# Performance work log

Measured on AMD Instinct MI355X. Metric: run time of the kernel, lower is better.

The kernel has to match this reference:

```python
import jax, jax.numpy as jnp
import numpy as np

# Dims: B=batch, S=max_input_len (memory), T=max_output_len-1 (decode steps),
# V=vocab, E=embedding_dim, U=dec_units, M=encoder/memory feature dim (=U here).

def setup_inputs() -> dict:
    B, S, T, V, E, U, M = 64, 1024, 511, 1024, 512, 1024, 1024
    key = jax.random.key(0)
    ks = jax.random.split(key, 16)
    sc = 0.02
    return {
        "tokens": jax.random.randint(ks[0], (B, T), 0, V),
        "memory": jax.random.normal(ks[1], (B, S, M), jnp.float32),
        "enc_h": jax.random.normal(ks[2], (B, U), jnp.float32) * 0.1,
        "enc_c": jax.random.normal(ks[3], (B, U), jnp.float32) * 0.1,
        "emb": jax.random.normal(ks[4], (V, E), jnp.float32) * sc,
        # LSTM cell: input = concat(embedded token, prev attention) -> E+U
        "Wk": jax.random.normal(ks[5], (E + U, 4 * U), jnp.float32) * sc,
        "Wr": jax.random.normal(ks[6], (U, 4 * U), jnp.float32) * sc,
        "b": jnp.zeros((4 * U,), jnp.float32),
        # Bahdanau attention: memory layer, query layer, score vector v
        "Wm": jax.random.normal(ks[7], (M, U), jnp.float32) * sc,
        "Wq": jax.random.normal(ks[8], (U, U), jnp.float32) * sc,
        "v": jax.random.normal(ks[9], (U,), jnp.float32) * sc,
        # attention_layer (Dense, no bias): concat(cell_out, context) -> U
        "Wa": jax.random.normal(ks[10], (U + M, U), jnp.float32) * sc,
        # output projection fc
        "Wfc": jax.random.normal(ks[11], (U, V), jnp.float32) * sc,
        "bfc": jnp.zeros((V,), jnp.float32),
    }


def reference(tokens, memory, enc_h, enc_c, emb, Wk, Wr, b, Wm, Wq, v, Wa, Wfc, bfc):
    B, U = enc_h.shape
    # Precompute attention keys once (memory_layer applied to memory): [B,S,U]
    keys = jnp.einsum('bsm,mu->bsu', memory, Wm)
    # Embedded decoder inputs, time-major for scan: [T,B,E]
    xseq = jnp.transpose(emb[tokens], (1, 0, 2))
    attn0 = jnp.zeros((B, U), memory.dtype)

    def step(carry, x_t):
        h, c, attn = carry
        # AttentionWrapper: cell input = concat(input, prev attention)
        z = jnp.concatenate([x_t, attn], axis=-1) @ Wk + h @ Wr + b
        i, f, g, o = jnp.split(z, 4, axis=-1)  # keras gate order i,f,c,o
        i = jax.nn.sigmoid(i)
        f = jax.nn.sigmoid(f)
        g = jnp.tanh(g)
        o = jax.nn.sigmoid(o)
        c_new = f * c + i * g
        h_new = o * jnp.tanh(c_new)
        # Bahdanau additive score: v^T tanh(W_q h + keys) -> [B,S]
        q = h_new @ Wq
        score = jnp.einsum('bsu,u->bs', jnp.tanh(q[:, None, :] + keys), v)
        alig = jax.nn.softmax(score, axis=-1)  # full-length memory mask (all valid)
        ctx = jnp.einsum('bs,bsm->bm', alig, memory)
        # attention_layer (no bias, no activation)
        attn_new = jnp.concatenate([h_new, ctx], axis=-1) @ Wa
        # output_attention=True: fc applied to attention output
        out = attn_new @ Wfc + bfc
        return (h_new, c_new, attn_new), out

    _, outs = jax.lax.scan(step, (enc_h, enc_c, attn0), xseq)
    return jnp.transpose(outs, (1, 0, 2))  # [B,T,V] rnn_output logits
```

## Files before the change

kernel.cpp:

```cpp
#include <hip/hip_runtime.h>
#include <stdint.h>

#define BB 64
#define SS 1024
#define TT 511
#define EE 512
#define UU 1024
#define G4 4096

typedef __bf16 bf16x8 __attribute__((ext_vector_type(8)));
typedef float  f32x4  __attribute__((ext_vector_type(4)));
typedef unsigned short u16x8 __attribute__((ext_vector_type(8)));

__device__ __forceinline__ float bf2f_lo(unsigned int u) {
    union { unsigned int i; float f; } w; w.i = u << 16; return w.f;
}
__device__ __forceinline__ float bf2f_hi(unsigned int u) {
    union { unsigned int i; float f; } w; w.i = u & 0xFFFF0000u; return w.f;
}
__device__ __forceinline__ unsigned short f2bf(float f) {
    union { float f; unsigned int i; } w; w.f = f;
    return (unsigned short)((w.i + 0x7FFFu + ((w.i >> 16) & 1u)) >> 16);
}
__device__ __forceinline__ float bfu2f(unsigned short u) {
    union { unsigned int i; float f; } w; w.i = ((unsigned int)u) << 16; return w.f;
}
__device__ __forceinline__ float fast_tanh(float x) {
    float e = __expf(2.0f * x);
    return 1.0f - 2.0f / (e + 1.0f);
}
__device__ __forceinline__ float sigmoidf_(float x) {
    return 1.0f / (1.0f + __expf(-x));
}

__device__ __forceinline__ int frag_slot(int m, int k, int KT, int hl) {
    return ((((m >> 4) * KT + (k >> 5)) * 2 + hl) * 64
            + ((m & 15) + (((k >> 3) & 3) << 4))) * 8 + (k & 7);
}

__device__ __forceinline__ f32x4 mfma16(bf16x8 a, bf16x8 b, f32x4 c) {
    return __builtin_amdgcn_mfma_f32_16x16x32_bf16(a, b, c, 0, 0, 0);
}

__global__ void k_cvt(const float4* __restrict__ src, ushort4* __restrict__ dst, int n4)
{
    int idx = blockIdx.x * 256 + threadIdx.x;
    for (int i = idx; i < n4; i += (int)gridDim.x * 256) {
        float4 f = src[i];
        ushort4 o;
        o.x = f2bf(f.x); o.y = f2bf(f.y); o.z = f2bf(f.z); o.w = f2bf(f.w);
        dst[i] = o;
    }
}

template<int OUTBF16>
__global__ __launch_bounds__(256) void k_mm1024(const float* __restrict__ A,
                                                const float* __restrict__ W,
                                                unsigned short* __restrict__ obf,
                                                float* __restrict__ of32)
{
    __shared__ __align__(16) float As[32][68];
    __shared__ __align__(16) float Ws[32][72];
    const int tid = threadIdx.x;
    const int tx = tid & 15, ty = tid >> 4;
    const int r0 = blockIdx.y * 64;
    const int c0 = blockIdx.x * 64;
    float acc[4][4] = {};
    const int am = tid >> 2, akq = tid & 3;
    const int wc4 = (tid & 15) * 4, wk0 = tid >> 4;
    for (int k0 = 0; k0 < 1024; k0 += 32) {
        const float* p = A + (size_t)(r0 + am) * 1024 + k0 + 8 * akq;
        float4 x0 = *(const float4*)p;
        float4 x1 = *(const float4*)(p + 4);
        As[8*akq+0][am] = x0.x; As[8*akq+1][am] = x0.y; As[8*akq+2][am] = x0.z; As[8*akq+3][am] = x0.w;
        As[8*akq+4][am] = x1.x; As[8*akq+5][am] = x1.y; As[8*akq+6][am] = x1.z; As[8*akq+7][am] = x1.w;
        #pragma unroll
        for (int j = 0; j < 2; ++j) {
            const int kk = wk0 + 16 * j;
            *(float4*)&Ws[kk][wc4] = *(const float4*)&W[(size_t)(k0 + kk) * 1024 + c0 + wc4];
        }
        __syncthreads();
        #pragma unroll
        for (int kk = 0; kk < 32; ++kk) {
            float4 a4 = *(const float4*)&As[kk][4 * ty];
            float4 w4 = *(const float4*)&Ws[kk][4 * tx];
            const float aa[4] = {a4.x, a4.y, a4.z, a4.w};
            const float ww[4] = {w4.x, w4.y, w4.z, w4.w};
            #pragma unroll
            for (int i = 0; i < 4; ++i)
                #pragma unroll
                for (int j = 0; j < 4; ++j)
                    acc[i][j] += aa[i] * ww[j];
        }
        __syncthreads();
    }
    #pragma unroll
    for (int i = 0; i < 4; ++i)
        #pragma unroll
        for (int j = 0; j < 4; ++j) {
            const size_t o = (size_t)(r0 + 4*ty + i) * 1024 + c0 + 4*tx + j;
            if (OUTBF16) obf[o] = f2bf(acc[i][j]);
            else         of32[o] = acc[i][j];
        }
}

__global__ void k_packw(const float* __restrict__ W1, const float* __restrict__ W2,
                        int split, int nmode, int KT, int s1, int s2,
                        unsigned short* __restrict__ dst)
{
    const int gid = blockIdx.x * 256 + threadIdx.x;
    const int lane = gid & 63;
    const int rest = gid >> 6;
    const int kt = rest % KT, nt = rest / KT;
    const int n = nt * 16 + (lane & 15);
    const int k0 = kt * 32 + (((lane >> 4) & 3) << 3);
    u16x8 hi, lo;
    #pragma unroll
    for (int j = 0; j < 8; ++j) {
        const int k = k0 + j;
        float f;
        if (nmode) f = (n < split) ? W1[(size_t)k * s1 + n] : W2[(size_t)k * s2 + (n - split)];
        else       f = (k < split) ? W1[(size_t)k * s1 + n] : W2[(size_t)(k - split) * s2 + n];
        hi[j] = f2bf(f);
        lo[j] = f2bf(f - bfu2f(hi[j]));
    }
    u16x8* d8 = (u16x8*)dst;
    d8[((nt * KT + kt) * 2 + 0) * 64 + lane] = hi;
    d8[((nt * KT + kt) * 2 + 1) * 64 + lane] = lo;
}

__global__ void k_init2(const float* __restrict__ enc_h, const float* __restrict__ enc_c,
                        const float* __restrict__ emb, const int* __restrict__ tokens,
                        float* __restrict__ c, unsigned short* __restrict__ Az)
{
    const int idx = blockIdx.x * 256 + threadIdx.x;
    const int b = idx >> 10, u = idx & 1023;
    c[idx] = enc_c[idx];
    const float hv = enc_h[idx];
    const unsigned short hh = f2bf(hv);
    const unsigned short hl = f2bf(hv - bfu2f(hh));
    Az[frag_slot(b, 1536 + u, 80, 0)] = hh;
    Az[frag_slot(b, 1536 + u, 80, 1)] = hl;
    Az[frag_slot(b, 512 + u, 80, 0)] = 0;
    Az[frag_slot(b, 512 + u, 80, 1)] = 0;
    if (u < EE) {
        const int tok = tokens[b * TT];
        const float v = emb[(size_t)tok * EE + u];
        const unsigned short eh = f2bf(v);
        Az[frag_slot(b, u, 80, 0)] = eh;
        Az[frag_slot(b, u, 80, 1)] = f2bf(v - bfu2f(eh));
    }
}

__global__ __launch_bounds__(256, 4) void k_mfma_z(const unsigned short* __restrict__ Azp,
                                                   const unsigned short* __restrict__ Bpp,
                                                   float* __restrict__ zpart)
{
    __shared__ float red[4][16][64];
    const int lane = threadIdx.x & 63, w = threadIdx.x >> 6;
    const int nt = blockIdx.x;
    const int g  = blockIdx.y;
    const bf16x8* A = (const bf16x8*)Azp;
    const bf16x8* B = (const bf16x8*)Bpp;
    f32x4 acc[4] = {{0.f,0.f,0.f,0.f},{0.f,0.f,0.f,0.f},{0.f,0.f,0.f,0.f},{0.f,0.f,0.f,0.f}};
    const int kt0 = g * 20 + w * 5;
    #pragma unroll
    for (int kk = 0; kk < 5; ++kk) {
        const int kt = kt0 + kk;
        const bf16x8 bh = B[((nt * 80 + kt) * 2 + 0) * 64 + lane];
        const bf16x8 bl = B[((nt * 80 + kt) * 2 + 1) * 64 + lane];
        #pragma unroll
        for (int m = 0; m < 4; ++m) {
            const bf16x8 ah = A[((m * 80 + kt) * 2 + 0) * 64 + lane];
            const bf16x8 al = A[((m * 80 + kt) * 2 + 1) * 64 + lane];
            acc[m] = mfma16(al, bh, acc[m]);
            acc[m] = mfma16(ah, bl, acc[m]);
            acc[m] = mfma16(ah, bh, acc[m]);
        }
    }
    #pragma unroll
    for (int m = 0; m < 4; ++m)
        #pragma unroll
        for (int r = 0; r < 4; ++r)
            red[w][m * 4 + r][lane] = acc[m][r];
    __syncthreads();
    const int m = w;
    float* Z = zpart + (size_t)g * BB * G4;
    const int col = nt * 16 + (lane & 15);
    const int rbase = (lane >> 4) * 4;
    #pragma unroll
    for (int r = 0; r < 4; ++r) {
        const float s = red[0][m*4+r][lane] + red[1][m*4+r][lane]
                      + red[2][m*4+r][lane] + red[3][m*4+r][lane];
        Z[(size_t)(m * 16 + rbase + r) * G4 + col] = s;
    }
}

__global__ __launch_bounds__(256, 4) void k_mfma_q(const unsigned short* __restrict__ Aqp,
                                                   const unsigned short* __restrict__ Bpp,
                                                   float* __restrict__ qpart)
{
    __shared__ float red[4][16][64];
    const int lane = threadIdx.x & 63, w = threadIdx.x >> 6;
    const int nt = blockIdx.x;
    const int g  = blockIdx.y;
    const bf16x8* A = (const bf16x8*)Aqp;
    const bf16x8* B = (const bf16x8*)Bpp;
    f32x4 acc[4] = {{0.f,0.f,0.f,0.f},{0.f,0.f,0.f,0.f},{0.f,0.f,0.f,0.f},{0.f,0.f,0.f,0.f}};
    const int kt0 = g * 8 + w * 2;
    #pragma unroll
    for (int kk = 0; kk < 2; ++kk) {
        const int kt = kt0 + kk;
        const bf16x8 bh = B[((nt * 32 + kt) * 2 + 0) * 64 + lane];
        const bf16x8 bl = B[((nt * 32 + kt) * 2 + 1) * 64 + lane];
        #pragma unroll
        for (int m = 0; m < 4; ++m) {
            const bf16x8 ah = A[((m * 32 + kt) * 2 + 0) * 64 + lane];
            const bf16x8 al = A[((m * 32 + kt) * 2 + 1) * 64 + lane];
            acc[m] = mfma16(al, bh, acc[m]);
            acc[m] = mfma16(ah, bl, acc[m]);
            acc[m] = mfma16(ah, bh, acc[m]);
        }
    }
    #pragma unroll
    for (int m = 0; m < 4; ++m)
        #pragma unroll
        for (int r = 0; r < 4; ++r)
            red[w][m * 4 + r][lane] = acc[m][r];
    __syncthreads();
    const int m = w;
    float* Q = qpart + (size_t)g * BB * UU;
    const int col = nt * 16 + (lane & 15);
    const int rbase = (lane >> 4) * 4;
    #pragma unroll
    for (int r = 0; r < 4; ++r) {
        const float s = red[0][m*4+r][lane] + red[1][m*4+r][lane]
                      + red[2][m*4+r][lane] + red[3][m*4+r][lane];
        Q[(size_t)(m * 16 + rbase + r) * UU + col] = s;
    }
}

__global__ __launch_bounds__(512, 2) void k_mfma_comb(const unsigned short* __restrict__ Aap,
                                                      const unsigned short* __restrict__ Bpp,
                                                      unsigned short* __restrict__ Az,
                                                      float* __restrict__ out,
                                                      const float* __restrict__ bfc, int t)
{
    __shared__ float red[8][16][64];
    const int lane = threadIdx.x & 63, w = threadIdx.x >> 6;
    const int nt = blockIdx.x;
    const bf16x8* A = (const bf16x8*)Aap;
    const bf16x8* B = (const bf16x8*)Bpp;
    f32x4 acc[4] = {{0.f,0.f,0.f,0.f},{0.f,0.f,0.f,0.f},{0.f,0.f,0.f,0.f},{0.f,0.f,0.f,0.f}};
    const int kt0 = w * 8;
    #pragma unroll
    for (int kk = 0; kk < 8; ++kk) {
        const int kt = kt0 + kk;
        const bf16x8 bh = B[((nt * 64 + kt) * 2 + 0) * 64 + lane];
        const bf16x8 bl = B[((nt * 64 + kt) * 2 + 1) * 64 + lane];
        #pragma unroll
        for (int m = 0; m < 4; ++m) {
            const bf16x8 ah = A[((m * 64 + kt) * 2 + 0) * 64 + lane];
            const bf16x8 al = A[((m * 64 + kt) * 2 + 1) * 64 + lane];
            acc[m] = mfma16(al, bh, acc[m]);
            acc[m] = mfma16(ah, bl, acc[m]);
            acc[m] = mfma16(ah, bh, acc[m]);
        }
    }
    #pragma unroll
    for (int m = 0; m < 4; ++m)
        #pragma unroll
        for (int r = 0; r < 4; ++r)
            red[w][m * 4 + r][lane] = acc[m][r];
    __syncthreads();
    if (w >= 4) return;
    const int m = w;
    const int n = nt * 16 + (lane & 15);
    const int rbase = (lane >> 4) * 4;
    #pragma unroll
    for (int r = 0; r < 4; ++r) {
        float s = 0.f;
        #pragma unroll
        for (int ww = 0; ww < 8; ++ww) s += red[ww][m*4+r][lane];
        const int row = m * 16 + rbase + r;
        if (n < 1024) {
            const unsigned short hh = f2bf(s);
            Az[frag_slot(row, 512 + n, 80, 0)] = hh;
            Az[frag_slot(row, 512 + n, 80, 1)] = f2bf(s - bfu2f(hh));
        } else {
            const int col = n - 1024;
            out[((size_t)row * TT + t) * 1024 + col] = s + bfc[col];
        }
    }
}

__global__ void k_gates2(const float* __restrict__ zpart, const float* __restrict__ bias,
                         float* __restrict__ c, unsigned short* __restrict__ Aq,
                         unsigned short* __restrict__ Aa2, unsigned short* __restrict__ Az,
                         const float* __restrict__ emb, const int* __restrict__ tokens,
                         int tnext)
{
    const int idx = blockIdx.x * 256 + threadIdx.x;
    if (idx < BB * UU) {
        const int b = idx >> 10, u = idx & 1023;
        float zi = 0.f, zf = 0.f, zg = 0.f, zo = 0.f;
        #pragma unroll
        for (int p = 0; p < 4; ++p) {
            const float* zp = zpart + ((size_t)p * BB + b) * G4;
            zi += zp[u]; zf += zp[u + 1024]; zg += zp[u + 2048]; zo += zp[u + 3072];
        }
        const float i_ = sigmoidf_(zi + bias[u]);
        const float f_ = sigmoidf_(zf + bias[u + 1024]);
        const float g_ = fast_tanh(zg + bias[u + 2048]);
        const float o_ = sigmoidf_(zo + bias[u + 3072]);
        const float cn = f_ * c[idx] + i_ * g_;
        c[idx] = cn;
        const float hv = o_ * fast_tanh(cn);
        const unsigned short hh = f2bf(hv);
        const unsigned short hl = f2bf(hv - bfu2f(hh));
        Aq [frag_slot(b, u,        32, 0)] = hh;  Aq [frag_slot(b, u,        32, 1)] = hl;
        Aa2[frag_slot(b, u,        64, 0)] = hh;  Aa2[frag_slot(b, u,        64, 1)] = hl;
        Az [frag_slot(b, 1536 + u, 80, 0)] = hh;  Az [frag_slot(b, 1536 + u, 80, 1)] = hl;
    } else if (tnext < TT) {
        const int r = idx - BB * UU;
        const int lane = r & 63;
        const int kt = (r >> 6) & 15;
        const int mrep = r >> 10;
        const int bb = mrep * 16 + (lane & 15);
        const int k0 = kt * 32 + (((lane >> 4) & 3) << 3);
        const int tok = tokens[bb * TT + tnext];
        const float* e = emb + (size_t)tok * EE + k0;
        const float4 x0 = *(const float4*)e;
        const float4 x1 = *(const float4*)(e + 4);
        const float f[8] = {x0.x, x0.y, x0.z, x0.w, x1.x, x1.y, x1.z, x1.w};
        u16x8 hi, lo;
        #pragma unroll
        for (int j = 0; j < 8; ++j) {
            hi[j] = f2bf(f[j]);
            lo[j] = f2bf(f[j] - bfu2f(hi[j]));
        }
        u16x8* A8 = (u16x8*)Az;
        A8[((mrep * 80 + kt) * 2 + 0) * 64 + lane] = hi;
        A8[((mrep * 80 + kt) * 2 + 1) * 64 + lane] = lo;
    }
}

__global__ void k_packctx(const float* __restrict__ ctxpart, const float* __restrict__ denompart,
                          unsigned short* __restrict__ Aa2)
{
    __shared__ float rdsh;
    const int idx = blockIdx.x * 256 + threadIdx.x;
    const int b = idx >> 10, u = idx & 1023;
    if (threadIdx.x == 0) {
        float d = 0.f;
        #pragma unroll
        for (int ch = 0; ch < 16; ++ch) d += denompart[ch * BB + b];
        rdsh = 1.0f / d;
    }
    float v = 0.f;
    #pragma unroll
    for (int ch = 0; ch < 16; ++ch) v += ctxpart[((size_t)ch * BB + b) * UU + u];
    __syncthreads();
    v *= rdsh;
    const unsigned short hh = f2bf(v);
    Aa2[frag_slot(b, 1024 + u, 64, 0)] = hh;
    Aa2[frag_slot(b, 1024 + u, 64, 1)] = f2bf(v - bfu2f(hh));
}

template<int BF16>
__global__ __launch_bounds__(256) void k_attn(const unsigned short* __restrict__ keys,
        const void* __restrict__ mem, const float* __restrict__ qpart,
        const float* __restrict__ vvec, float* __restrict__ denompart,
        float* __restrict__ ctxpart)
{
    __shared__ float qs[1024];
    __shared__ float vs[1024];
    __shared__ float es[64];
    __shared__ float dsum[4];
    __shared__ __align__(16) float cred[128][8];
    const int tid = threadIdx.x;
    const int bid = blockIdx.x;
    const int b = bid >> 4, chunk = bid & 15;
    const int s0 = chunk * 64;
    for (int i = tid; i < UU; i += 256) {
        const size_t o = (size_t)b * UU + i;
        qs[i] = qpart[o] + qpart[o + (size_t)BB * UU]
              + qpart[o + 2 * (size_t)BB * UU] + qpart[o + 3 * (size_t)BB * UU];
        vs[i] = vvec[i];
    }
    __syncthreads();
    const int lane = tid & 63;
    const int w = tid >> 6;
    float qv[16], vv[16];
    #pragma unroll
    for (int j = 0; j < 2; ++j)
        #pragma unroll
        for (int i = 0; i < 8; ++i) {
            qv[8*j + i] = qs[8*lane + 512*j + i];
            vv[8*j + i] = vs[8*lane + 512*j + i];
        }
    float wsum = 0.f;
    for (int it = 0; it < 8; ++it) {
        const int sl = w * 16 + it * 2;
        const unsigned short* kp0 = keys + ((size_t)(b * SS + s0 + sl) << 10);
        const unsigned short* kp1 = kp0 + 1024;
        const uint4 r00 = *(const uint4*)&kp0[8*lane];
        const uint4 r01 = *(const uint4*)&kp0[8*lane + 512];
        const uint4 r10 = *(const uint4*)&kp1[8*lane];
        const uint4 r11 = *(const uint4*)&kp1[8*lane + 512];
        float acc0 = 0.f, acc1 = 0.f;
        {
            const uint4 rr[2] = {r00, r01};
            #pragma unroll
            for (int j = 0; j < 2; ++j) {
                float kx[8];
                kx[0] = bf2f_lo(rr[j].x); kx[1] = bf2f_hi(rr[j].x);
                kx[2] = bf2f_lo(rr[j].y); kx[3] = bf2f_hi(rr[j].y);
                kx[4] = bf2f_lo(rr[j].z); kx[5] = bf2f_hi(rr[j].z);
                kx[6] = bf2f_lo(rr[j].w); kx[7] = bf2f_hi(rr[j].w);
                #pragma unroll
                for (int i = 0; i < 8; ++i)
                    acc0 += vv[8*j + i] * fast_tanh(qv[8*j + i] + kx[i]);
            }
        }
        {
            const uint4 rr[2] = {r10, r11};
            #pragma unroll
            for (int j = 0; j < 2; ++j) {
                float kx[8];
                kx[0] = bf2f_lo(rr[j].x); kx[1] = bf2f_hi(rr[j].x);
                kx[2] = bf2f_lo(rr[j].y); kx[3] = bf2f_hi(rr[j].y);
                kx[4] = bf2f_lo(rr[j].z); kx[5] = bf2f_hi(rr[j].z);
                kx[6] = bf2f_lo(rr[j].w); kx[7] = bf2f_hi(rr[j].w);
                #pragma unroll
                for (int i = 0; i < 8; ++i)
                    acc1 += vv[8*j + i] * fast_tanh(qv[8*j + i] + kx[i]);
            }
        }
        #pragma unroll
        for (int m = 32; m >= 1; m >>= 1) {
            acc0 += __shfl_xor(acc0, m, 64);
            acc1 += __shfl_xor(acc1, m, 64);
        }
        if (lane == 0) {
            const float e0 = __expf(acc0);
            const float e1 = __expf(acc1);
            es[sl] = e0;
            es[sl + 1] = e1;
            wsum += e0 + e1;
        }
    }
    if (lane == 0) dsum[w] = wsum;
    __syncthreads();
    if (tid == 0)
        denompart[chunk * BB + b] = dsum[0] + dsum[1] + dsum[2] + dsum[3];
    const int m8 = (tid & 127) * 8;
    const int shalf = tid >> 7;
    float a[8] = {};
    #pragma unroll 8
    for (int i = 0; i < 32; ++i) {
        const int sl = shalf * 32 + i;
        const float wgt = es[sl];
        const size_t base = ((size_t)(b * SS + s0 + sl) << 10) + m8;
        if (BF16) {
            uint4 u = *(const uint4*)((const unsigned short*)mem + base);
            a[0] += wgt * bf2f_lo(u.x); a[1] += wgt * bf2f_hi(u.x);
            a[2] += wgt * bf2f_lo(u.y); a[3] += wgt * bf2f_hi(u.y);
            a[4] += wgt * bf2f_lo(u.z); a[5] += wgt * bf2f_hi(u.z);
            a[6] += wgt * bf2f_lo(u.w); a[7] += wgt * bf2f_hi(u.w);
        } else {
            const float* fp = (const float*)mem + base;
            const float4 f0 = *(const float4*)fp;
            const float4 f1 = *(const float4*)(fp + 4);
            a[0] += wgt * f0.x; a[1] += wgt * f0.y; a[2] += wgt * f0.z; a[3] += wgt * f0.w;
            a[4] += wgt * f1.x; a[5] += wgt * f1.y; a[6] += wgt * f1.z; a[7] += wgt * f1.w;
        }
    }
    if (shalf) {
        #pragma unroll
        for (int j = 0; j < 8; ++j) cred[tid - 128][j] = a[j];
    }
    __syncthreads();
    if (!shalf) {
        float* cp = ctxpart + ((size_t)chunk * BB + b) * UU + m8;
        float4 o0, o1;
        o0.x = a[0] + cred[tid][0]; o0.y = a[1] + cred[tid][1];
        o0.z = a[2] + cred[tid][2]; o0.w = a[3] + cred[tid][3];
        o1.x = a[4] + cred[tid][4]; o1.y = a[5] + cred[tid][5];
        o1.z = a[6] + cred[tid][6]; o1.w = a[7] + cred[tid][7];
        *(float4*)cp = o0;
        *(float4*)(cp + 4) = o1;
    }
}

extern "C" void kernel_launch(void* const* d_in, const int* in_sizes, int n_in,
                              void* d_out, int out_size, void* d_ws, size_t ws_size,
                              hipStream_t stream)
{
    const int*   tokens = (const int*)d_in[0];
    const float* memory = (const float*)d_in[1];
    const float* enc_h  = (const float*)d_in[2];
    const float* enc_c  = (const float*)d_in[3];
    const float* emb    = (const float*)d_in[4];
    const float* Wk     = (const float*)d_in[5];
    const float* Wr     = (const float*)d_in[6];
    const float* bias   = (const float*)d_in[7];
    const float* Wm     = (const float*)d_in[8];
    const float* Wq     = (const float*)d_in[9];
    const float* vvec   = (const float*)d_in[10];
    const float* Wa     = (const float*)d_in[11];
    const float* Wfc    = (const float*)d_in[12];
    const float* bfc    = (const float*)d_in[13];
    float* out = (float*)d_out;

    char* ws = (char*)d_ws;
    size_t off = 0;
    auto take = [&](size_t bytes) -> char* {
        char* p = ws + off;
        off = (off + bytes + 255) & ~(size_t)255;
        return p;
    };
    unsigned short* keys   = (unsigned short*)take((size_t)BB * SS * UU * 2);
    unsigned short* WkrP   = (unsigned short*)take((size_t)256 * 80 * 2 * 64 * 16);
    unsigned short* WcombP = (unsigned short*)take((size_t)128 * 64 * 2 * 64 * 16);
    unsigned short* WqP    = (unsigned short*)take((size_t)64  * 32 * 2 * 64 * 16);
    float* wafc  = (float*)take((size_t)2048 * 1024 * 4);
    float* zpart = (float*)take((size_t)4 * BB * G4 * 4);
    float* qpart = (float*)take((size_t)4 * BB * UU * 4);
    float* c     = (float*)take((size_t)BB * UU * 4);
    float* ctxpart   = (float*)take((size_t)16 * BB * UU * 4);
    float* denompart = (float*)take((size_t)16 * BB * 4);
    unsigned short* Az  = (unsigned short*)take((size_t)4 * 80 * 2 * 64 * 16);
    unsigned short* Aq  = (unsigned short*)take((size_t)4 * 32 * 2 * 64 * 16);
    unsigned short* Aa2 = (unsigned short*)take((size_t)4 * 64 * 2 * 64 * 16);
    const bool planA = (off + (size_t)BB * SS * UU * 2) <= ws_size;
    unsigned short* membf = planA ? (unsigned short*)take((size_t)BB * SS * UU * 2) : nullptr;

    k_init2<<<dim3(256), dim3(256), 0, stream>>>(enc_h, enc_c, emb, tokens, c, Az);
    if (planA)
        k_cvt<<<dim3(4096), dim3(256), 0, stream>>>((const float4*)memory, (ushort4*)membf,
                                                    (BB * SS * UU) / 4);
    k_mm1024<1><<<dim3(16, 1024), dim3(256), 0, stream>>>(memory, Wm, keys, nullptr);
    k_mm1024<0><<<dim3(16, 32),   dim3(256), 0, stream>>>(Wa, Wfc, nullptr, wafc);
    k_packw<<<dim3(5120), dim3(256), 0, stream>>>(Wk, Wr, 1536, 0, 80, 4096, 4096, WkrP);
    k_packw<<<dim3(512),  dim3(256), 0, stream>>>(Wq, Wq, 1 << 30, 0, 32, 1024, 1024, WqP);
    k_packw<<<dim3(2048), dim3(256), 0, stream>>>(Wa, wafc, 1024, 1, 64, 1024, 1024, WcombP);

    for (int t = 0; t < TT; ++t) {
        k_mfma_z<<<dim3(256, 4), dim3(256), 0, stream>>>(Az, WkrP, zpart);
        k_gates2<<<dim3(272), dim3(256), 0, stream>>>(zpart, bias, c, Aq, Aa2, Az,
                                                      emb, tokens, t + 1);
        k_mfma_q<<<dim3(64, 4), dim3(256), 0, stream>>>(Aq, WqP, qpart);
        if (planA)
            k_attn<1><<<dim3(1024), dim3(256), 0, stream>>>(keys, membf, qpart, vvec,
                                                            denompart, ctxpart);
        else
            k_attn<0><<<dim3(1024), dim3(256), 0, stream>>>(keys, memory, qpart, vvec,
                                                            denompart, ctxpart);
        k_packctx<<<dim3(256), dim3(256), 0, stream>>>(ctxpart, denompart, Aa2);
        k_mfma_comb<<<dim3(128), dim3(512), 0, stream>>>(Aa2, WcombP, Az, out, bfc, t);
    }
}
```

Measured before the change: 53.42 ms.

## Fold attention-output into LSTM weights, merge z and q GEMMs, MFMA keys

Precomputes Wa·Wk[attn part] so each step's attention contribution to the LSTM gates comes straight from the combine GEMM, which removes the attention vector as an LSTM input. It also merges the per-step z GEMM (embedding and h) with the query GEMM into one launch. This drops a kernel launch per step and shrinks the recurrent K dimension from 1536+512 to 1536. The keys precompute now uses a bf16 MFMA kernel on the converted memory instead of the fp32 SIMT GEMM, and scratch buffers are reused for the converted memory. The fold adds extra precompute and changes numerical rounding, since the folded weights are split into two bf16 parts.

```diff
diff --git a/kernel.cpp b/kernel.cpp
--- a/kernel.cpp
+++ b/kernel.cpp
@@ -7,6 +7,8 @@
 #define EE 512
 #define UU 1024
 #define G4 4096
+#define QZKT 48
+#define CBKT 64
 
 typedef __bf16 bf16x8 __attribute__((ext_vector_type(8)));
 typedef float  f32x4  __attribute__((ext_vector_type(4)));
@@ -54,10 +56,10 @@
 }
 
 template<int OUTBF16>
-__global__ __launch_bounds__(256) void k_mm1024(const float* __restrict__ A,
-                                                const float* __restrict__ W,
-                                                unsigned short* __restrict__ obf,
-                                                float* __restrict__ of32)
+__global__ __launch_bounds__(256) void k_mmN(const float* __restrict__ A,
+                                             const float* __restrict__ W,
+                                             unsigned short* __restrict__ obf,
+                                             float* __restrict__ of32, int N)
 {
     __shared__ __align__(16) float As[32][68];
     __shared__ __align__(16) float Ws[32][72];
@@ -77,7 +79,7 @@
         #pragma unroll
         for (int j = 0; j < 2; ++j) {
             const int kk = wk0 + 16 * j;
-            *(float4*)&Ws[kk][wc4] = *(const float4*)&W[(size_t)(k0 + kk) * 1024 + c0 + wc4];
+            *(float4*)&Ws[kk][wc4] = *(const float4*)&W[(size_t)(k0 + kk) * N + c0 + wc4];
         }
         __syncthreads();
         #pragma unroll
@@ -98,7 +100,7 @@
     for (int i = 0; i < 4; ++i)
         #pragma unroll
         for (int j = 0; j < 4; ++j) {
-            const size_t o = (size_t)(r0 + 4*ty + i) * 1024 + c0 + 4*tx + j;
+            const size_t o = (size_t)(r0 + 4*ty + i) * N + c0 + 4*tx + j;
             if (OUTBF16) obf[o] = f2bf(acc[i][j]);
             else         of32[o] = acc[i][j];
         }
@@ -129,50 +131,129 @@
     d8[((nt * KT + kt) * 2 + 1) * 64 + lane] = lo;
 }
 
+__global__ void k_packqz(const float* __restrict__ Wk, const float* __restrict__ Wr,
+                         const float* __restrict__ Wq, unsigned short* __restrict__ dst)
+{
+    const int gid = blockIdx.x * 256 + threadIdx.x;
+    const int lane = gid & 63;
+    const int rest = gid >> 6;
+    const int kt = rest % QZKT, nt = rest / QZKT;
+    const int n = nt * 16 + (lane & 15);
+    const int k0 = kt * 32 + (((lane >> 4) & 3) << 3);
+    u16x8 hi, lo;
+    #pragma unroll
+    for (int j = 0; j < 8; ++j) {
+        const int k = k0 + j;
+        float f;
+        if (n < 4096) f = (k < 512) ? Wk[(size_t)k * 4096 + n] : Wr[(size_t)(k - 512) * 4096 + n];
+        else          f = (k < 512) ? 0.f : Wq[(size_t)(k - 512) * 1024 + (n - 4096)];
+        hi[j] = f2bf(f);
+        lo[j] = f2bf(f - bfu2f(hi[j]));
+    }
+    u16x8* d8 = (u16x8*)dst;
+    d8[((nt * QZKT + kt) * 2 + 0) * 64 + lane] = hi;
+    d8[((nt * QZKT + kt) * 2 + 1) * 64 + lane] = lo;
+}
+
 __global__ void k_init2(const float* __restrict__ enc_h, const float* __restrict__ enc_c,
                         const float* __restrict__ emb, const int* __restrict__ tokens,
-                        float* __restrict__ c, unsigned short* __restrict__ Az)
+                        float* __restrict__ c, unsigned short* __restrict__ Aqz,
+                        float* __restrict__ zattn)
 {
     const int idx = blockIdx.x * 256 + threadIdx.x;
     const int b = idx >> 10, u = idx & 1023;
     c[idx] = enc_c[idx];
     const float hv = enc_h[idx];
     const unsigned short hh = f2bf(hv);
-    const unsigned short hl = f2bf(hv - bfu2f(hh));
-    Az[frag_slot(b, 1536 + u, 80, 0)] = hh;
-    Az[frag_slot(b, 1536 + u, 80, 1)] = hl;
-    Az[frag_slot(b, 512 + u, 80, 0)] = 0;
-    Az[frag_slot(b, 512 + u, 80, 1)] = 0;
+    Aqz[frag_slot(b, 512 + u, QZKT, 0)] = hh;
+    Aqz[frag_slot(b, 512 + u, QZKT, 1)] = f2bf(hv - bfu2f(hh));
     if (u < EE) {
         const int tok = tokens[b * TT];
         const float v = emb[(size_t)tok * EE + u];
         const unsigned short eh = f2bf(v);
-        Az[frag_slot(b, u, 80, 0)] = eh;
-        Az[frag_slot(b, u, 80, 1)] = f2bf(v - bfu2f(eh));
-    }
-}
-
-__global__ __launch_bounds__(256, 4) void k_mfma_z(const unsigned short* __restrict__ Azp,
-                                                   const unsigned short* __restrict__ Bpp,
-                                                   float* __restrict__ zpart)
+        Aqz[frag_slot(b, u, QZKT, 0)] = eh;
+        Aqz[frag_slot(b, u, QZKT, 1)] = f2bf(v - bfu2f(eh));
+    }
+    #pragma unroll
+    for (int j = 0; j < 4; ++j) zattn[idx + j * 65536] = 0.f;
+}
+
+__global__ __launch_bounds__(256, 2) void k_keys_mfma(const unsigned short* __restrict__ membf,
+        const unsigned short* __restrict__ WmP, unsigned short* __restrict__ keys)
+{
+    __shared__ bf16x8 Bs[32][64];
+    const int tid = threadIdx.x, lane = tid & 63, w = tid >> 6;
+    const int bx = blockIdx.x;
+    const int by = blockIdx.y;
+    const bf16x8* mb = (const bf16x8*)membf;
+    const bf16x8* B8 = (const bf16x8*)WmP;
+    f32x4 acc[2][16];
+    const f32x4 z4 = {0.f, 0.f, 0.f, 0.f};
+    #pragma unroll
+    for (int i = 0; i < 2; ++i)
+        #pragma unroll
+        for (int j = 0; j < 16; ++j) acc[i][j] = z4;
+    const int r0a = by * 128 + (w * 2) * 16 + (lane & 15);
+    const int r0b = r0a + 16;
+    const int kq = lane >> 4;
+    for (int kt = 0; kt < 32; ++kt) {
+        const bf16x8 ah0 = mb[(size_t)r0a * 128 + kt * 4 + kq];
+        const bf16x8 ah1 = mb[(size_t)r0b * 128 + kt * 4 + kq];
+        __syncthreads();
+        #pragma unroll
+        for (int j = 0; j < 8; ++j) {
+            const int slot = tid + j * 256;
+            const int frag = slot >> 6, l2 = slot & 63;
+            const int ntl = frag >> 1, hl = frag & 1;
+            Bs[frag][l2] = B8[((((size_t)bx * 16 + ntl) * 32 + kt) * 2 + hl) * 64 + l2];
+        }
+        __syncthreads();
+        #pragma unroll
+        for (int nt = 0; nt < 16; ++nt) {
+            const bf16x8 bh = Bs[nt * 2][lane];
+            const bf16x8 bl = Bs[nt * 2 + 1][lane];
+            acc[0][nt] = mfma16(ah0, bl, acc[0][nt]);
+            acc[0][nt] = mfma16(ah0, bh, acc[0][nt]);
+            acc[1][nt] = mfma16(ah1, bl, acc[1][nt]);
+            acc[1][nt] = mfma16(ah1, bh, acc[1][nt]);
+        }
+    }
+    const int rbase = (lane >> 4) * 4;
+    const int c16 = lane & 15;
+    #pragma unroll
+    for (int mi = 0; mi < 2; ++mi)
+        #pragma unroll
+        for (int nt = 0; nt < 16; ++nt)
+            #pragma unroll
+            for (int r = 0; r < 4; ++r) {
+                const int row = by * 128 + (w * 2 + mi) * 16 + rbase + r;
+                const int col = bx * 256 + nt * 16 + c16;
+                keys[(size_t)row * 1024 + col] = f2bf(acc[mi][nt][r]);
+            }
+}
+
+__global__ __launch_bounds__(256, 4) void k_mfma_qz(const unsigned short* __restrict__ Ap,
+                                                    const unsigned short* __restrict__ Bp,
+                                                    float* __restrict__ zpart2,
+                                                    float* __restrict__ qpart)
 {
     __shared__ float red[4][16][64];
     const int lane = threadIdx.x & 63, w = threadIdx.x >> 6;
     const int nt = blockIdx.x;
     const int g  = blockIdx.y;
-    const bf16x8* A = (const bf16x8*)Azp;
-    const bf16x8* B = (const bf16x8*)Bpp;
+    const bf16x8* A = (const bf16x8*)Ap;
+    const bf16x8* B = (const bf16x8*)Bp;
     f32x4 acc[4] = {{0.f,0.f,0.f,0.f},{0.f,0.f,0.f,0.f},{0.f,0.f,0.f,0.f},{0.f,0.f,0.f,0.f}};
-    const int kt0 = g * 20 + w * 5;
-    #pragma unroll
-    for (int kk = 0; kk < 5; ++kk) {
+    const int kt0 = g * 12 + w * 3;
+    #pragma unroll
+    for (int kk = 0; kk < 3; ++kk) {
         const int kt = kt0 + kk;
-        const bf16x8 bh = B[((nt * 80 + kt) * 2 + 0) * 64 + lane];
-        const bf16x8 bl = B[((nt * 80 + kt) * 2 + 1) * 64 + lane];
+        const bf16x8 bh = B[((nt * QZKT + kt) * 2 + 0) * 64 + lane];
+        const bf16x8 bl = B[((nt * QZKT + kt) * 2 + 1) * 64 + lane];
         #pragma unroll
         for (int m = 0; m < 4; ++m) {
-            const bf16x8 ah = A[((m * 80 + kt) * 2 + 0) * 64 + lane];
-            const bf16x8 al = A[((m * 80 + kt) * 2 + 1) * 64 + lane];
+            const bf16x8 ah = A[((m * QZKT + kt) * 2 + 0) * 64 + lane];
+            const bf16x8 al = A[((m * QZKT + kt) * 2 + 1) * 64 + lane];
             acc[m] = mfma16(al, bh, acc[m]);
             acc[m] = mfma16(ah, bl, acc[m]);
             acc[m] = mfma16(ah, bh, acc[m]);
@@ -185,83 +266,40 @@
             red[w][m * 4 + r][lane] = acc[m][r];
     __syncthreads();
     const int m = w;
-    float* Z = zpart + (size_t)g * BB * G4;
-    const int col = nt * 16 + (lane & 15);
+    const int c16 = lane & 15;
     const int rbase = (lane >> 4) * 4;
     #pragma unroll
     for (int r = 0; r < 4; ++r) {
         const float s = red[0][m*4+r][lane] + red[1][m*4+r][lane]
                       + red[2][m*4+r][lane] + red[3][m*4+r][lane];
-        Z[(size_t)(m * 16 + rbase + r) * G4 + col] = s;
-    }
-}
-
-__global__ __launch_bounds__(256, 4) void k_mfma_q(const unsigned short* __restrict__ Aqp,
-                                                   const unsigned short* __restrict__ Bpp,
-                                                   float* __restrict__ qpart)
-{
-    __shared__ float red[4][16][64];
-    const int lane = threadIdx.x & 63, w = threadIdx.x >> 6;
-    const int nt = blockIdx.x;
-    const int g  = blockIdx.y;
-    const bf16x8* A = (const bf16x8*)Aqp;
-    const bf16x8* B = (const bf16x8*)Bpp;
-    f32x4 acc[4] = {{0.f,0.f,0.f,0.f},{0.f,0.f,0.f,0.f},{0.f,0.f,0.f,0.f},{0.f,0.f,0.f,0.f}};
-    const int kt0 = g * 8 + w * 2;
-    #pragma unroll
-    for (int kk = 0; kk < 2; ++kk) {
-        const int kt = kt0 + kk;
-        const bf16x8 bh = B[((nt * 32 + kt) * 2 + 0) * 64 + lane];
-        const bf16x8 bl = B[((nt * 32 + kt) * 2 + 1) * 64 + lane];
-        #pragma unroll
-        for (int m = 0; m < 4; ++m) {
-            const bf16x8 ah = A[((m * 32 + kt) * 2 + 0) * 64 + lane];
-            const bf16x8 al = A[((m * 32 + kt) * 2 + 1) * 64 + lane];
-            acc[m] = mfma16(al, bh, acc[m]);
-            acc[m] = mfma16(ah, bl, acc[m]);
-            acc[m] = mfma16(ah, bh, acc[m]);
-        }
-    }
-    #pragma unroll
-    for (int m = 0; m < 4; ++m)
-        #pragma unroll
-        for (int r = 0; r < 4; ++r)
-            red[w][m * 4 + r][lane] = acc[m][r];
-    __syncthreads();
-    const int m = w;
-    float* Q = qpart + (size_t)g * BB * UU;
-    const int col = nt * 16 + (lane & 15);
-    const int rbase = (lane >> 4) * 4;
-    #pragma unroll
-    for (int r = 0; r < 4; ++r) {
-        const float s = red[0][m*4+r][lane] + red[1][m*4+r][lane]
-                      + red[2][m*4+r][lane] + red[3][m*4+r][lane];
-        Q[(size_t)(m * 16 + rbase + r) * UU + col] = s;
-    }
-}
-
-__global__ __launch_bounds__(512, 2) void k_mfma_comb(const unsigned short* __restrict__ Aap,
-                                                      const unsigned short* __restrict__ Bpp,
-                                                      unsigned short* __restrict__ Az,
-                                                      float* __restrict__ out,
-                                                      const float* __restrict__ bfc, int t)
+        const int row = m * 16 + rbase + r;
+        if (nt < 256) zpart2[(size_t)g * BB * G4 + (size_t)row * G4 + nt * 16 + c16] = s;
+        else          qpart [(size_t)g * BB * UU + (size_t)row * UU + (nt - 256) * 16 + c16] = s;
+    }
+}
+
+__global__ __launch_bounds__(512, 2) void k_mfma_comb2(const unsigned short* __restrict__ Ap,
+                                                       const unsigned short* __restrict__ Bp,
+                                                       float* __restrict__ zattn,
+                                                       float* __restrict__ out,
+                                                       const float* __restrict__ bfc, int t)
 {
     __shared__ float red[8][16][64];
     const int lane = threadIdx.x & 63, w = threadIdx.x >> 6;
     const int nt = blockIdx.x;
-    const bf16x8* A = (const bf16x8*)Aap;
-    const bf16x8* B = (const bf16x8*)Bpp;
+    const bf16x8* A = (const bf16x8*)Ap;
+    const bf16x8* B = (const bf16x8*)Bp;
     f32x4 acc[4] = {{0.f,0.f,0.f,0.f},{0.f,0.f,0.f,0.f},{0.f,0.f,0.f,0.f},{0.f,0.f,0.f,0.f}};
     const int kt0 = w * 8;
     #pragma unroll
     for (int kk = 0; kk < 8; ++kk) {
         const int kt = kt0 + kk;
-        const bf16x8 bh = B[((nt * 64 + kt) * 2 + 0) * 64 + lane];
-        const bf16x8 bl = B[((nt * 64 + kt) * 2 + 1) * 64 + lane];
+        const bf16x8 bh = B[((nt * CBKT + kt) * 2 + 0) * 64 + lane];
+        const bf16x8 bl = B[((nt * CBKT + kt) * 2 + 1) * 64 + lane];
         #pragma unroll
         for (int m = 0; m < 4; ++m) {
-            const bf16x8 ah = A[((m * 64 + kt) * 2 + 0) * 64 + lane];
-            const bf16x8 al = A[((m * 64 + kt) * 2 + 1) * 64 + lane];
+            const bf16x8 ah = A[((m * CBKT + kt) * 2 + 0) * 64 + lane];
+            const bf16x8 al = A[((m * CBKT + kt) * 2 + 1) * 64 + lane];
             acc[m] = mfma16(al, bh, acc[m]);
             acc[m] = mfma16(ah, bl, acc[m]);
             acc[m] = mfma16(ah, bh, acc[m]);
@@ -275,7 +313,7 @@
     __syncthreads();
     if (w >= 4) return;
     const int m = w;
-    const int n = nt * 16 + (lane & 15);
+    const int c16 = lane & 15;
     const int rbase = (lane >> 4) * 4;
     #pragma unroll
     for (int r = 0; r < 4; ++r) {
@@ -283,30 +321,31 @@
         #pragma unroll
         for (int ww = 0; ww < 8; ++ww) s += red[ww][m*4+r][lane];
         const int row = m * 16 + rbase + r;
-        if (n < 1024) {
-            const unsigned short hh = f2bf(s);
-            Az[frag_slot(row, 512 + n, 80, 0)] = hh;
-            Az[frag_slot(row, 512 + n, 80, 1)] = f2bf(s - bfu2f(hh));
+        if (nt < 64) {
+            const int col = nt * 16 + c16;
+            out[((size_t)row * TT + t) * 1024 + col] = s + bfc[col];
         } else {
-            const int col = n - 1024;
-            out[((size_t)row * TT + t) * 1024 + col] = s + bfc[col];
-        }
-    }
-}
-
-__global__ void k_gates2(const float* __restrict__ zpart, const float* __restrict__ bias,
-                         float* __restrict__ c, unsigned short* __restrict__ Aq,
-                         unsigned short* __restrict__ Aa2, unsigned short* __restrict__ Az,
+            zattn[(size_t)row * G4 + (nt - 64) * 16 + c16] = s;
+        }
+    }
+}
+
+__global__ void k_gates3(const float* __restrict__ zpart2, const float* __restrict__ zattn,
+                         const float* __restrict__ bias, float* __restrict__ c,
+                         unsigned short* __restrict__ Aqz, unsigned short* __restrict__ Acomb,
                          const float* __restrict__ emb, const int* __restrict__ tokens,
                          int tnext)
 {
     const int idx = blockIdx.x * 256 + threadIdx.x;
     if (idx < BB * UU) {
         const int b = idx >> 10, u = idx & 1023;
-        float zi = 0.f, zf = 0.f, zg = 0.f, zo = 0.f;
+        float zi = zattn[(size_t)b * G4 + u];
+        float zf = zattn[(size_t)b * G4 + u + 1024];
+        float zg = zattn[(size_t)b * G4 + u + 2048];
+        float zo = zattn[(size_t)b * G4 + u + 3072];
         #pragma unroll
         for (int p = 0; p < 4; ++p) {
-            const float* zp = zpart + ((size_t)p * BB + b) * G4;
+            const float* zp = zpart2 + ((size_t)p * BB + b) * G4;
             zi += zp[u]; zf += zp[u + 1024]; zg += zp[u + 2048]; zo += zp[u + 3072];
         }
         const float i_ = sigmoidf_(zi + bias[u]);
@@ -318,9 +357,8 @@
         const float hv = o_ * fast_tanh(cn);
         const unsigned short hh = f2bf(hv);
         const unsigned short hl = f2bf(hv - bfu2f(hh));
-        Aq [frag_slot(b, u,        32, 0)] = hh;  Aq [frag_slot(b, u,        32, 1)] = hl;
-        Aa2[frag_slot(b, u,        64, 0)] = hh;  Aa2[frag_slot(b, u,        64, 1)] = hl;
-        Az [frag_slot(b, 1536 + u, 80, 0)] = hh;  Az [frag_slot(b, 1536 + u, 80, 1)] = hl;
+        Aqz  [frag_slot(b, 512 + u, QZKT, 0)] = hh;  Aqz  [frag_slot(b, 512 + u, QZKT, 1)] = hl;
+        Acomb[frag_slot(b, u,       CBKT, 0)] = hh;  Acomb[frag_slot(b, u,       CBKT, 1)] = hl;
     } else if (tnext < TT) {
         const int r = idx - BB * UU;
         const int lane = r & 63;
@@ -339,14 +377,14 @@
             hi[j] = f2bf(f[j]);
             lo[j] = f2bf(f[j] - bfu2f(hi[j]));
         }
-        u16x8* A8 = (u16x8*)Az;
-        A8[((mrep * 80 + kt) * 2 + 0) * 64 + lane] = hi;
-        A8[((mrep * 80 + kt) * 2 + 1) * 64 + lane] = lo;
-    }
-}
-
-__global__ void k_packctx(const float* __restrict__ ctxpart, const float* __restrict__ denompart,
-                          unsigned short* __restrict__ Aa2)
+        u16x8* A8 = (u16x8*)Aqz;
+        A8[((mrep * QZKT + kt) * 2 + 0) * 64 + lane] = hi;
+        A8[((mrep * QZKT + kt) * 2 + 1) * 64 + lane] = lo;
+    }
+}
+
+__global__ void k_packctx2(const float* __restrict__ ctxpart, const float* __restrict__ denompart,
+                           unsigned short* __restrict__ Acomb)
 {
     __shared__ float rdsh;
     const int idx = blockIdx.x * 256 + threadIdx.x;
@@ -363,8 +401,8 @@
     __syncthreads();
     v *= rdsh;
     const unsigned short hh = f2bf(v);
-    Aa2[frag_slot(b, 1024 + u, 64, 0)] = hh;
-    Aa2[frag_slot(b, 1024 + u, 64, 1)] = f2bf(v - bfu2f(hh));
+    Acomb[frag_slot(b, 1024 + u, CBKT, 0)] = hh;
+    Acomb[frag_slot(b, 1024 + u, CBKT, 1)] = f2bf(v - bfu2f(hh));
 }
 
 template<int BF16>
@@ -520,44 +558,51 @@
         off = (off + bytes + 255) & ~(size_t)255;
         return p;
     };
-    unsigned short* keys   = (unsigned short*)take((size_t)BB * SS * UU * 2);
-    unsigned short* WkrP   = (unsigned short*)take((size_t)256 * 80 * 2 * 64 * 16);
-    unsigned short* WcombP = (unsigned short*)take((size_t)128 * 64 * 2 * 64 * 16);
-    unsigned short* WqP    = (unsigned short*)take((size_t)64  * 32 * 2 * 64 * 16);
-    float* wafc  = (float*)take((size_t)2048 * 1024 * 4);
-    float* zpart = (float*)take((size_t)4 * BB * G4 * 4);
-    float* qpart = (float*)take((size_t)4 * BB * UU * 4);
-    float* c     = (float*)take((size_t)BB * UU * 4);
+    unsigned short* keys    = (unsigned short*)take((size_t)BB * SS * UU * 2);
+    unsigned short* WqzP    = (unsigned short*)take((size_t)320 * QZKT * 2 * 64 * 16);
+    unsigned short* Wcomb2P = (unsigned short*)take((size_t)320 * CBKT * 2 * 64 * 16);
+    unsigned short* WmP     = (unsigned short*)take((size_t)64 * 32 * 2 * 64 * 16);
+    float* zpart2 = (float*)take((size_t)4 * BB * G4 * 4);
+    float* qpart  = (float*)take((size_t)4 * BB * UU * 4);
+    float* c      = (float*)take((size_t)BB * UU * 4);
     float* ctxpart   = (float*)take((size_t)16 * BB * UU * 4);
     float* denompart = (float*)take((size_t)16 * BB * 4);
-    unsigned short* Az  = (unsigned short*)take((size_t)4 * 80 * 2 * 64 * 16);
-    unsigned short* Aq  = (unsigned short*)take((size_t)4 * 32 * 2 * 64 * 16);
-    unsigned short* Aa2 = (unsigned short*)take((size_t)4 * 64 * 2 * 64 * 16);
-    const bool planA = (off + (size_t)BB * SS * UU * 2) <= ws_size;
-    unsigned short* membf = planA ? (unsigned short*)take((size_t)BB * SS * UU * 2) : nullptr;
-
-    k_init2<<<dim3(256), dim3(256), 0, stream>>>(enc_h, enc_c, emb, tokens, c, Az);
-    if (planA)
+    float* zattn  = (float*)take((size_t)BB * G4 * 4);
+    unsigned short* Aqz   = (unsigned short*)take((size_t)4 * QZKT * 2 * 64 * 16);
+    unsigned short* Acomb = (unsigned short*)take((size_t)4 * CBKT * 2 * 64 * 16);
+    char* scratch = take((size_t)2048 * 1024 * 4 + (size_t)2048 * 4096 * 4);
+    float* wafc = (float*)scratch;
+    float* wk2f = (float*)(scratch + (size_t)2048 * 1024 * 4);
+    const size_t scratch_off = (size_t)(scratch - ws);
+    const bool planA = (scratch_off + (size_t)BB * SS * UU * 2 + 256) <= ws_size;
+    unsigned short* membf = planA ? (unsigned short*)scratch : nullptr;
+
+    k_init2<<<dim3(256), dim3(256), 0, stream>>>(enc_h, enc_c, emb, tokens, c, Aqz, zattn);
+    k_mmN<0><<<dim3(16, 32), dim3(256), 0, stream>>>(Wa, Wfc, nullptr, wafc, 1024);
+    k_mmN<0><<<dim3(64, 32), dim3(256), 0, stream>>>(Wa, Wk + (size_t)512 * 4096, nullptr, wk2f, 4096);
+    k_packw<<<dim3(5120), dim3(256), 0, stream>>>(wafc, wk2f, 1024, 1, CBKT, 1024, 4096, Wcomb2P);
+    k_packqz<<<dim3(3840), dim3(256), 0, stream>>>(Wk, Wr, Wq, WqzP);
+    if (planA) {
+        k_packw<<<dim3(512), dim3(256), 0, stream>>>(Wm, Wm, 1 << 30, 0, 32, 1024, 1024, WmP);
         k_cvt<<<dim3(4096), dim3(256), 0, stream>>>((const float4*)memory, (ushort4*)membf,
                                                     (BB * SS * UU) / 4);
-    k_mm1024<1><<<dim3(16, 1024), dim3(256), 0, stream>>>(memory, Wm, keys, nullptr);
-    k_mm1024<0><<<dim3(16, 32),   dim3(256), 0, stream>>>(Wa, Wfc, nullptr, wafc);
-    k_packw<<<dim3(5120), dim3(256), 0, stream>>>(Wk, Wr, 1536, 0, 80, 4096, 4096, WkrP);
-    k_packw<<<dim3(512),  dim3(256), 0, stream>>>(Wq, Wq, 1 << 30, 0, 32, 1024, 1024, WqP);
-    k_packw<<<dim3(2048), dim3(256), 0, stream>>>(Wa, wafc, 1024, 1, 64, 1024, 1024, WcombP);
+        k_keys_mfma<<<dim3(4, 512), dim3(256), 0, stream>>>(membf, WmP, keys);
+    } else {
+        k_mmN<1><<<dim3(16, 1024), dim3(256), 0, stream>>>(memory, Wm, keys, nullptr, 1024);
+    }
+    k_mfma_qz<<<dim3(320, 4), dim3(256), 0, stream>>>(Aqz, WqzP, zpart2, qpart);
 
     for (int t = 0; t < TT; ++t) {
-        k_mfma_z<<<dim3(256, 4), dim3(256), 0, stream>>>(Az, WkrP, zpart);
-        k_gates2<<<dim3(272), dim3(256), 0, stream>>>(zpart, bias, c, Aq, Aa2, Az,
+        k_gates3<<<dim3(272), dim3(256), 0, stream>>>(zpart2, zattn, bias, c, Aqz, Acomb,
                                                       emb, tokens, t + 1);
-        k_mfma_q<<<dim3(64, 4), dim3(256), 0, stream>>>(Aq, WqP, qpart);
+        k_mfma_qz<<<dim3(320, 4), dim3(256), 0, stream>>>(Aqz, WqzP, zpart2, qpart);
         if (planA)
             k_attn<1><<<dim3(1024), dim3(256), 0, stream>>>(keys, membf, qpart, vvec,
                                                             denompart, ctxpart);
         else
             k_attn<0><<<dim3(1024), dim3(256), 0, stream>>>(keys, memory, qpart, vvec,
                                                             denompart, ctxpart);
-        k_packctx<<<dim3(256), dim3(256), 0, stream>>>(ctxpart, denompart, Aa2);
-        k_mfma_comb<<<dim3(128), dim3(512), 0, stream>>>(Aa2, WcombP, Az, out, bfc, t);
-    }
-}
+        k_packctx2<<<dim3(256), dim3(256), 0, stream>>>(ctxpart, denompart, Acomb);
+        k_mfma_comb2<<<dim3(320), dim3(512), 0, stream>>>(Acomb, Wcomb2P, zattn, out, bfc, t);
+    }
+}
```

Result: faster. 51.63 ms (-3.3%).
